# Kernel optimization log

Hardware: AMD Instinct MI355X
Metric: run time of the kernel (lower is better)

## Reference

```python
import jax, jax.numpy as jnp
import numpy as np

B, T, F_IN = 32, 2000, 256
HIDDEN, OUT = 1024, 256
TAU, DT, G = 0.01, 0.001, 1.2
HID_NOISE, OUT_NOISE = 0.05, 0.5
SPARSITY = 0.1


def setup_inputs() -> dict:
    key = jax.random.key(0)
    k_in, k_wr_n, k_wr_s, k_wi, k_wf, k_wo, k_xh, k_xo = jax.random.split(key, 8)
    inputs = jax.random.normal(k_in, (B, T, F_IN), dtype=jnp.float32)
    # recurrent kernel: sparse normal init (flax Dense kernel shape = (in, out))
    std = np.sqrt(1.0 / (SPARSITY * HIDDEN)).astype(np.float32)
    Wr = jax.random.normal(k_wr_n, (HIDDEN, HIDDEN), dtype=jnp.float32) * std
    Wr = Wr * jax.random.bernoulli(k_wr_s, 1.0 - SPARSITY, (HIDDEN, HIDDEN))
    # input and feedback kernels: uniform in [-1, 1)
    Wi = jax.random.uniform(k_wi, (F_IN, HIDDEN), dtype=jnp.float32, minval=-1.0, maxval=1.0)
    Wf = jax.random.uniform(k_wf, (OUT, HIDDEN), dtype=jnp.float32, minval=-1.0, maxval=1.0)
    # readout kernel (zeros_init in source; small random here for nontrivial signal)
    Wo = jax.random.normal(k_wo, (HIDDEN, OUT), dtype=jnp.float32) * 0.01
    # split_rngs={'reservoir': False} => same noise reused at every timestep
    xi_hidden = jax.random.uniform(k_xh, (B, HIDDEN), dtype=jnp.float32, minval=-HID_NOISE, maxval=HID_NOISE)
    xi_output = jax.random.uniform(k_xo, (B, OUT), dtype=jnp.float32, minval=-OUT_NOISE, maxval=OUT_NOISE)
    return {"inputs": inputs, "Wr": Wr, "Wi": Wi, "Wf": Wf, "Wo": Wo,
            "xi_hidden": xi_hidden, "xi_output": xi_output}


def reference(inputs, Wr, Wi, Wf, Wo, xi_hidden, xi_output):
    # inputs: [B, T, F_in]; scan over time with carry u: [B, H]
    x_t_first = jnp.swapaxes(inputs, 0, 1)  # [T, B, F_in]
    u0 = jnp.zeros((inputs.shape[0], Wr.shape[0]), dtype=inputs.dtype)

    def step(u, x):
        r = jnp.tanh(u) + xi_hidden                       # [B, H]
        z = r @ Wo + xi_output                            # [B, O]
        du = G * (r @ Wr) + x @ Wi + z @ Wf               # [B, H]
        u_new = u + DT * (du - u) / TAU                   # Euler update
        return u_new, z

    _, outputs = jax.lax.scan(step, u0, x_t_first)        # [T, B, O]
    return jnp.swapaxes(outputs, 0, 1)                    # [B, T, O]
```

## Files before the change

### kernel.cpp

```cpp
#include <hip/hip_runtime.h>
#include <math.h>

#define NB   32
#define NT   2000
#define NFIN 256
#define NH   1024
#define NOUT 256
#define KC   1280
#define GRID 256
#define BLK  256
#define HALF 128

#define WC_STR 12
#define OFF_WC   0
#define OFF_WOT  (OFF_WC + KC * WC_STR)
#define XS_STR   20
#define OFF_XS   (OFF_WOT + 2 * NH)
#define PD_STR   68
#define OFF_PD   (OFF_XS + NFIN * XS_STR)
#define LDS_FLOATS (OFF_PD + 160 * PD_STR)
#define LDS_BYTES  (LDS_FLOATS * 4)

__global__ __launch_bounds__(256) void init_wcomb(
    const float* __restrict__ Wr, const float* __restrict__ Wi,
    const float* __restrict__ Wf, const float* __restrict__ Wo,
    float* __restrict__ Wcb, float* __restrict__ Wot)
{
    __shared__ float wo_s[NOUT];
    const int k   = blockIdx.x;
    const int tid = threadIdx.x;
    float acc[4];
    if (k < NH) {
        wo_s[tid] = Wo[k * NOUT + tid];
        __syncthreads();
        Wot[(size_t)tid * NH + k] = wo_s[tid];
#pragma unroll
        for (int jj = 0; jj < 4; ++jj)
            acc[jj] = 1.2f * Wr[k * NH + jj * 256 + tid];
        for (int o = 0; o < NOUT; ++o) {
            const float w = wo_s[o];
#pragma unroll
            for (int jj = 0; jj < 4; ++jj)
                acc[jj] = fmaf(w, Wf[o * NH + jj * 256 + tid], acc[jj]);
        }
    } else {
        const int k2 = k - NH;
#pragma unroll
        for (int jj = 0; jj < 4; ++jj)
            acc[jj] = Wi[k2 * NH + jj * 256 + tid];
    }
#pragma unroll
    for (int jj = 0; jj < 4; ++jj) {
        const int j = jj * 256 + tid;
        Wcb[(size_t)(j >> 3) * (KC * 8) + k * 8 + (j & 7)] = acc[jj];
    }
}

__global__ __launch_bounds__(256) void init_state(
    const float* __restrict__ Wf, const float* __restrict__ xi_o,
    const float* __restrict__ xi_h,
    float* __restrict__ c_km, float* __restrict__ xih_km,
    float* __restrict__ r0, unsigned* __restrict__ bar)
{
    __shared__ float xo_s[NOUT];
    const int b   = blockIdx.x;
    const int tid = threadIdx.x;
    if (b == 0) bar[tid] = 0u;
    xo_s[tid] = xi_o[b * NOUT + tid];
    __syncthreads();
    float acc[4] = {0.f, 0.f, 0.f, 0.f};
    for (int o = 0; o < NOUT; ++o) {
        const float x = xo_s[o];
#pragma unroll
        for (int jj = 0; jj < 4; ++jj)
            acc[jj] = fmaf(x, Wf[o * NH + jj * 256 + tid], acc[jj]);
    }
#pragma unroll
    for (int jj = 0; jj < 4; ++jj) {
        const int j = jj * 256 + tid;
        const float xh = xi_h[b * NH + j];
        c_km[j * NB + b]   = acc[jj];
        xih_km[j * NB + b] = xh;
        r0[j * NB + b]     = xh;
    }
}

extern "C" __global__ __launch_bounds__(BLK, 1) void reservoir_persistent(
    const float* __restrict__ x_all,
    const float* __restrict__ Wcb,
    const float* __restrict__ Wot,
    const float* __restrict__ c_km,
    const float* __restrict__ xih_km,
    const float* __restrict__ xi_o,
    float* __restrict__ r0, float* __restrict__ r1,
    float* __restrict__ out,
    unsigned* __restrict__ bar)
{
    extern __shared__ float sm[];
    float* Wc_s  = sm + OFF_WC;
    float* Wot_s = sm + OFF_WOT;
    float* x_s   = sm + OFF_XS;
    float* pd    = sm + OFF_PD;

    const int tid = threadIdx.x;
    const int blk = blockIdx.x;
    const int bg  = blk & 1;
    const int cg  = blk >> 1;
    const int b0  = bg * 16;
    const int j0  = cg * 8;
    const int zc0 = cg * 2;

    unsigned* cnt = bar + (bg << 6);
    unsigned* flg = bar + 128 + (bg << 6);

#pragma unroll
    for (int i = 0; i < 10; ++i) {
        const int q = tid + BLK * i;
        const int k = q >> 1, h = q & 1;
        const float4 w = *(const float4*)&Wcb[(size_t)cg * (KC * 8) + k * 8 + h * 4];
        *(float4*)&Wc_s[k * WC_STR + h * 4] = w;
    }
#pragma unroll
    for (int i = 0; i < 8; ++i) {
        const int idx = tid + BLK * i;
        Wot_s[idx] = Wot[(size_t)zc0 * NH + idx];
    }

    float u_reg = 0.f, c_reg = 0.f, xih_reg = 0.f;
    int ep_addr = 0;
    if (tid < 128) {
        const int j = j0 + (tid >> 4);
        const int b = b0 + (tid & 15);
        ep_addr = j * NB + b;
        c_reg   = c_km[ep_addr];
        xih_reg = xih_km[ep_addr];
    }
    float zxi = 0.f; size_t z_out_base = 0;
    if (tid >= 128 && tid < 160) {
        const int o2 = tid - 128;
        const int zc = zc0 + (o2 >> 4);
        const int zb = b0 + (o2 & 15);
        zxi = xi_o[zb * NOUT + zc];
        z_out_base = (size_t)zb * NT * NOUT + zc;
    }

    const int ks5 = tid >> 2;
    const int bq  = tid & 3;
    const int bb  = tid & 15;
    const int q2  = tid >> 4;

    const float* rcur = r0;
    float*       rnxt = r1;

    {
        const float* xp = x_all + ((size_t)(b0 + bb) * NT + 0) * NFIN;
#pragma unroll
        for (int i = 0; i < 4; ++i) {
            const int kk = (q2 + 16 * i) * 4;
            const float4 v = *(const float4*)&xp[kk];
            x_s[(kk + 0) * XS_STR + bb] = v.x;
            x_s[(kk + 1) * XS_STR + bb] = v.y;
            x_s[(kk + 2) * XS_STR + bb] = v.z;
            x_s[(kk + 3) * XS_STR + bb] = v.w;
        }
    }
    __syncthreads();

    for (int t = 0; t < NT; ++t) {
        float ad[8][4], az[2][4];
#pragma unroll
        for (int jj = 0; jj < 8; ++jj)
#pragma unroll
            for (int i = 0; i < 4; ++i) ad[jj][i] = 0.f;
#pragma unroll
        for (int jq = 0; jq < 2; ++jq)
#pragma unroll
            for (int i = 0; i < 4; ++i) az[jq][i] = 0.f;

        const float* rbase = rcur + b0 + bq * 4;
        float4 rq4[16];
#pragma unroll
        for (int p = 0; p < 16; ++p)
            rq4[p] = *(const float4*)(rbase + (size_t)(ks5 + (p << 6)) * NB);

#pragma unroll
        for (int m = 0; m < 16; ++m) {
            const int k = ks5 + (m << 6);
            const float4 a = rq4[m];
            const float4 w0 = *(const float4*)&Wc_s[k * WC_STR];
            const float4 w1 = *(const float4*)&Wc_s[k * WC_STR + 4];
            const float z0 = Wot_s[k], z1 = Wot_s[NH + k];
            const float av[4] = {a.x, a.y, a.z, a.w};
            const float wv[8] = {w0.x, w0.y, w0.z, w0.w, w1.x, w1.y, w1.z, w1.w};
#pragma unroll
            for (int i = 0; i < 4; ++i) {
#pragma unroll
                for (int jj = 0; jj < 8; ++jj)
                    ad[jj][i] = fmaf(av[i], wv[jj], ad[jj][i]);
                az[0][i] = fmaf(av[i], z0, az[0][i]);
                az[1][i] = fmaf(av[i], z1, az[1][i]);
            }
        }
#pragma unroll
        for (int m = 0; m < 4; ++m) {
            const int kk = ks5 + (m << 6);
            const int k  = kk + NH;
            const float4 a  = *(const float4*)&x_s[kk * XS_STR + bq * 4];
            const float4 w0 = *(const float4*)&Wc_s[k * WC_STR];
            const float4 w1 = *(const float4*)&Wc_s[k * WC_STR + 4];
            const float av[4] = {a.x, a.y, a.z, a.w};
            const float wv[8] = {w0.x, w0.y, w0.z, w0.w, w1.x, w1.y, w1.z, w1.w};
#pragma unroll
            for (int i = 0; i < 4; ++i)
#pragma unroll
                for (int jj = 0; jj < 8; ++jj)
                    ad[jj][i] = fmaf(av[i], wv[jj], ad[jj][i]);
        }

        const int tn = (t + 1 < NT) ? (t + 1) : (NT - 1);
        float4 xv[4];
        {
            const float* xp = x_all + ((size_t)(b0 + bb) * NT + tn) * NFIN;
#pragma unroll
            for (int i = 0; i < 4; ++i)
                xv[i] = *(const float4*)&xp[(q2 + 16 * i) * 4];
        }

#pragma unroll
        for (int jj = 0; jj < 8; ++jj)
#pragma unroll
            for (int i = 0; i < 4; ++i)
                pd[(jj * 16 + bq * 4 + i) * PD_STR + ks5] = ad[jj][i];
#pragma unroll
        for (int jq = 0; jq < 2; ++jq)
#pragma unroll
            for (int i = 0; i < 4; ++i)
                pd[(128 + jq * 16 + bq * 4 + i) * PD_STR + ks5] = az[jq][i];
        __syncthreads();

        if (tid < 160) {
            const float* row = &pd[tid * PD_STR];
            float4 s4 = make_float4(0.f, 0.f, 0.f, 0.f);
#pragma unroll
            for (int q = 0; q < 16; ++q) {
                const float4 v = *(const float4*)&row[q * 4];
                s4.x += v.x; s4.y += v.y; s4.z += v.z; s4.w += v.w;
            }
            const float s = (s4.x + s4.y) + (s4.z + s4.w);
            if (tid < 128) {
                const float un = 0.9f * u_reg + 0.1f * (s + c_reg);
                u_reg = un;
                rnxt[ep_addr] = tanhf(un) + xih_reg;
            } else {
                out[z_out_base + (size_t)t * NOUT] = s + zxi;
            }
        }

        {
#pragma unroll
            for (int i = 0; i < 4; ++i) {
                const int kk = (q2 + 16 * i) * 4;
                const float4 v = xv[i];
                x_s[(kk + 0) * XS_STR + bb] = v.x;
                x_s[(kk + 1) * XS_STR + bb] = v.y;
                x_s[(kk + 2) * XS_STR + bb] = v.z;
                x_s[(kk + 3) * XS_STR + bb] = v.w;
            }
        }
        __syncthreads();

        if (tid == 0) {
            __builtin_amdgcn_fence(__ATOMIC_RELEASE, "agent");
            const unsigned tgt = (unsigned)HALF * (unsigned)(t + 1);
            const unsigned old = __hip_atomic_fetch_add(cnt, 1u, __ATOMIC_RELAXED,
                                                        __HIP_MEMORY_SCOPE_AGENT);
            if (old == tgt - 1u) {
                __hip_atomic_store(flg, tgt, __ATOMIC_RELAXED,
                                   __HIP_MEMORY_SCOPE_AGENT);
            } else {
                while (__hip_atomic_load(flg, __ATOMIC_RELAXED,
                                         __HIP_MEMORY_SCOPE_AGENT) < tgt)
                    __builtin_amdgcn_s_sleep(2);
            }
            __builtin_amdgcn_fence(__ATOMIC_ACQUIRE, "agent");
        }
        __syncthreads();

        float* tmp = (float*)rcur; rcur = rnxt; rnxt = tmp;
    }
}

extern "C" void kernel_launch(void* const* d_in, const int* in_sizes, int n_in,
                              void* d_out, int out_size, void* d_ws, size_t ws_size,
                              hipStream_t stream)
{
    const float* inputs = (const float*)d_in[0];
    const float* Wr     = (const float*)d_in[1];
    const float* Wi     = (const float*)d_in[2];
    const float* Wf     = (const float*)d_in[3];
    const float* Wo     = (const float*)d_in[4];
    const float* xi_h   = (const float*)d_in[5];
    const float* xi_o   = (const float*)d_in[6];
    float* out = (float*)d_out;

    float* ws     = (float*)d_ws;
    float* Wcb    = ws;
    float* Wot    = Wcb + 128 * KC * 8;
    float* c_km   = Wot + NOUT * NH;
    float* xih_km = c_km + NH * NB;
    float* r0     = xih_km + NH * NB;
    float* r1     = r0 + NH * NB;
    unsigned* bar = (unsigned*)(r1 + NH * NB);

    (void)hipFuncSetAttribute((const void*)reservoir_persistent,
                              hipFuncAttributeMaxDynamicSharedMemorySize, LDS_BYTES);

    init_wcomb<<<KC, 256, 0, stream>>>(Wr, Wi, Wf, Wo, Wcb, Wot);
    init_state<<<NB, 256, 0, stream>>>(Wf, xi_o, xi_h, c_km, xih_km, r0, bar);

    void* args[] = {
        (void*)&inputs, (void*)&Wcb, (void*)&Wot, (void*)&c_km, (void*)&xih_km,
        (void*)&xi_o, (void*)&r0, (void*)&r1, (void*)&out, (void*)&bar
    };
    (void)hipLaunchCooperativeKernel((void*)reservoir_persistent,
                                     dim3(GRID), dim3(BLK), args, LDS_BYTES, stream);
}
```

Before: 17.36 ms.

## Replace barrier fences with cache-bypassing loads/stores and pipeline r-chunk waits

Drops the agent-scope release/acquire fences around the grid barrier. Instead the shared r state is written and read with cache-bypassing (sc0 sc1) global instructions, and the counter/flag barrier is restructured so that any waiter can publish the flag. The r loads are issued up front and consumed in four chunks with staged vmcnt waits so compute overlaps the load latency. The x-part operands are prefetched into registers while the barrier is pending, and the Wot layout is interleaved so the two output weights come from one paired load. The fence removal relies on inline-asm cache bypass for correctness, which is fragile and may break memory ordering.

Result: slower. 20.07 ms (+15.6%).

```diff
diff --git a/kernel.cpp b/kernel.cpp
--- a/kernel.cpp
+++ b/kernel.cpp
@@ -10,6 +10,8 @@
 #define GRID 256
 #define BLK  256
 #define HALF 128
+
+typedef float f32x4 __attribute__((ext_vector_type(4)));
 
 #define WC_STR 12
 #define OFF_WC   0
@@ -123,7 +125,7 @@
 #pragma unroll
     for (int i = 0; i < 8; ++i) {
         const int idx = tid + BLK * i;
-        Wot_s[idx] = Wot[(size_t)zc0 * NH + idx];
+        Wot_s[((idx & 1023) << 1) | (idx >> 10)] = Wot[(size_t)zc0 * NH + idx];
     }
 
     float u_reg = 0.f, c_reg = 0.f, xih_reg = 0.f;
@@ -166,50 +168,71 @@
     }
     __syncthreads();
 
-    for (int t = 0; t < NT; ++t) {
-        float ad[8][4], az[2][4];
-#pragma unroll
-        for (int jj = 0; jj < 8; ++jj)
-#pragma unroll
-            for (int i = 0; i < 4; ++i) ad[jj][i] = 0.f;
-#pragma unroll
-        for (int jq = 0; jq < 2; ++jq)
-#pragma unroll
-            for (int i = 0; i < 4; ++i) az[jq][i] = 0.f;
-
-        const float* rbase = rcur + b0 + bq * 4;
-        float4 rq4[16];
-#pragma unroll
-        for (int p = 0; p < 16; ++p)
-            rq4[p] = *(const float4*)(rbase + (size_t)(ks5 + (p << 6)) * NB);
-
-#pragma unroll
-        for (int m = 0; m < 16; ++m) {
-            const int k = ks5 + (m << 6);
-            const float4 a = rq4[m];
-            const float4 w0 = *(const float4*)&Wc_s[k * WC_STR];
-            const float4 w1 = *(const float4*)&Wc_s[k * WC_STR + 4];
-            const float z0 = Wot_s[k], z1 = Wot_s[NH + k];
-            const float av[4] = {a.x, a.y, a.z, a.w};
-            const float wv[8] = {w0.x, w0.y, w0.z, w0.w, w1.x, w1.y, w1.z, w1.w};
-#pragma unroll
-            for (int i = 0; i < 4; ++i) {
-#pragma unroll
-                for (int jj = 0; jj < 8; ++jj)
-                    ad[jj][i] = fmaf(av[i], wv[jj], ad[jj][i]);
-                az[0][i] = fmaf(av[i], z0, az[0][i]);
-                az[1][i] = fmaf(av[i], z1, az[1][i]);
-            }
-        }
+    float4 xa[4], wx0[4], wx1[4];
+    auto prefetch_xpart = [&]() {
 #pragma unroll
         for (int m = 0; m < 4; ++m) {
             const int kk = ks5 + (m << 6);
-            const int k  = kk + NH;
-            const float4 a  = *(const float4*)&x_s[kk * XS_STR + bq * 4];
-            const float4 w0 = *(const float4*)&Wc_s[k * WC_STR];
-            const float4 w1 = *(const float4*)&Wc_s[k * WC_STR + 4];
-            const float av[4] = {a.x, a.y, a.z, a.w};
-            const float wv[8] = {w0.x, w0.y, w0.z, w0.w, w1.x, w1.y, w1.z, w1.w};
+            xa[m]  = *(const float4*)&x_s[kk * XS_STR + bq * 4];
+            wx0[m] = *(const float4*)&Wc_s[(kk + NH) * WC_STR];
+            wx1[m] = *(const float4*)&Wc_s[(kk + NH) * WC_STR + 4];
+        }
+    };
+    prefetch_xpart();
+
+    for (int t = 0; t < NT; ++t) {
+        const float* rbase = rcur + b0 + bq * 4;
+        f32x4 rq4[16];
+#pragma unroll
+        for (int p = 0; p < 16; ++p) {
+            const float* ap = rbase + (size_t)(ks5 + (p << 6)) * NB;
+            asm volatile("global_load_dwordx4 %0, %1, off sc0 sc1"
+                         : "=v"(rq4[p]) : "v"(ap));
+        }
+
+        float ad[8][4], az[2][4];
+#pragma unroll
+        for (int jj = 0; jj < 8; ++jj)
+#pragma unroll
+            for (int i = 0; i < 4; ++i) ad[jj][i] = 0.f;
+#pragma unroll
+        for (int jq = 0; jq < 2; ++jq)
+#pragma unroll
+            for (int i = 0; i < 4; ++i) az[jq][i] = 0.f;
+
+#define RCHUNK(M0, M1, VW)                                                     \
+        asm volatile("s_waitcnt vmcnt(" #VW ")" ::: "memory");                 \
+        __builtin_amdgcn_sched_barrier(0);                                     \
+        _Pragma("unroll")                                                      \
+        for (int m = M0; m < M1; ++m) {                                        \
+            const int k = ks5 + (m << 6);                                      \
+            const f32x4 a = rq4[m];                                            \
+            const float4 w0 = *(const float4*)&Wc_s[k * WC_STR];               \
+            const float4 w1 = *(const float4*)&Wc_s[k * WC_STR + 4];           \
+            const float2 zz = *(const float2*)&Wot_s[k * 2];                   \
+            const float av[4] = {a[0], a[1], a[2], a[3]};                      \
+            const float wv[8] = {w0.x, w0.y, w0.z, w0.w,                       \
+                                 w1.x, w1.y, w1.z, w1.w};                      \
+            _Pragma("unroll")                                                  \
+            for (int i = 0; i < 4; ++i) {                                      \
+                _Pragma("unroll")                                              \
+                for (int jj = 0; jj < 8; ++jj)                                 \
+                    ad[jj][i] = fmaf(av[i], wv[jj], ad[jj][i]);                \
+                az[0][i] = fmaf(av[i], zz.x, az[0][i]);                        \
+                az[1][i] = fmaf(av[i], zz.y, az[1][i]);                        \
+            }                                                                  \
+        }
+        RCHUNK(0, 4, 12)
+        RCHUNK(4, 8, 8)
+        RCHUNK(8, 12, 4)
+        RCHUNK(12, 16, 0)
+#undef RCHUNK
+
+#pragma unroll
+        for (int m = 0; m < 4; ++m) {
+            const float av[4] = {xa[m].x, xa[m].y, xa[m].z, xa[m].w};
+            const float wv[8] = {wx0[m].x, wx0[m].y, wx0[m].z, wx0[m].w,
+                                 wx1[m].x, wx1[m].y, wx1[m].z, wx1[m].w};
 #pragma unroll
             for (int i = 0; i < 4; ++i)
 #pragma unroll
@@ -250,11 +273,16 @@
             if (tid < 128) {
                 const float un = 0.9f * u_reg + 0.1f * (s + c_reg);
                 u_reg = un;
-                rnxt[ep_addr] = tanhf(un) + xih_reg;
+                const float rv = tanhf(un) + xih_reg;
+                const float* sp = rnxt + ep_addr;
+                asm volatile("global_store_dword %0, %1, off sc0 sc1"
+                             :: "v"(sp), "v"(rv) : "memory");
             } else {
                 out[z_out_base + (size_t)t * NOUT] = s + zxi;
             }
         }
+
+        asm volatile("s_waitcnt vmcnt(0)" ::: "memory");
 
         {
 #pragma unroll
@@ -269,20 +297,24 @@
         }
         __syncthreads();
 
+        if (tid == 0)
+            __hip_atomic_fetch_add(cnt, 1u, __ATOMIC_RELAXED,
+                                   __HIP_MEMORY_SCOPE_AGENT);
+
+        prefetch_xpart();
+
         if (tid == 0) {
-            __builtin_amdgcn_fence(__ATOMIC_RELEASE, "agent");
             const unsigned tgt = (unsigned)HALF * (unsigned)(t + 1);
-            const unsigned old = __hip_atomic_fetch_add(cnt, 1u, __ATOMIC_RELAXED,
-                                                        __HIP_MEMORY_SCOPE_AGENT);
-            if (old == tgt - 1u) {
-                __hip_atomic_store(flg, tgt, __ATOMIC_RELAXED,
-                                   __HIP_MEMORY_SCOPE_AGENT);
-            } else {
-                while (__hip_atomic_load(flg, __ATOMIC_RELAXED,
-                                         __HIP_MEMORY_SCOPE_AGENT) < tgt)
-                    __builtin_amdgcn_s_sleep(2);
+            while (__hip_atomic_load(flg, __ATOMIC_RELAXED,
+                                     __HIP_MEMORY_SCOPE_AGENT) < tgt) {
+                if (__hip_atomic_load(cnt, __ATOMIC_RELAXED,
+                                      __HIP_MEMORY_SCOPE_AGENT) >= tgt) {
+                    __hip_atomic_store(flg, tgt, __ATOMIC_RELAXED,
+                                       __HIP_MEMORY_SCOPE_AGENT);
+                    break;
+                }
+                __builtin_amdgcn_s_sleep(2);
             }
-            __builtin_amdgcn_fence(__ATOMIC_ACQUIRE, "agent");
         }
         __syncthreads();
 
```

## Replace flat grid barrier with two-level tree barrier and split arrive/wait

Applied to the files above, without the earlier changes.

Swaps the single-counter atomic barrier per batch group for a two-level tree: 16 leaf counters of 8 blocks each feed a root counter, which sets a flag. The hidden-state and output stores now use system-coherent (sc0 sc1) global stores followed by a vmcnt wait instead of a release fence, and the arrive is issued before the x_s staging, so that staging overlaps the barrier latency. This aims to cut atomic contention and barrier latency on the per-timestep grid sync. The risks are memory-ordering correctness relying on the cache-bypass stores, and a larger barrier-initialisation footprint.

New measurement: 17.84 ms. 1.03x slower.

```diff
diff --git a/kernel.cpp b/kernel.cpp
--- a/kernel.cpp
+++ b/kernel.cpp
@@ -65,7 +65,7 @@
     __shared__ float xo_s[NOUT];
     const int b   = blockIdx.x;
     const int tid = threadIdx.x;
-    if (b == 0) bar[tid] = 0u;
+    if (tid < 32) bar[b * 32 + tid] = 0u;
     xo_s[tid] = xi_o[b * NOUT + tid];
     __syncthreads();
     float acc[4] = {0.f, 0.f, 0.f, 0.f};
@@ -109,9 +109,11 @@
     const int b0  = bg * 16;
     const int j0  = cg * 8;
     const int zc0 = cg * 2;
-
-    unsigned* cnt = bar + (bg << 6);
-    unsigned* flg = bar + 128 + (bg << 6);
+    const int lf  = cg >> 3;
+
+    unsigned* leaf = bar + (bg << 9) + (lf << 4);
+    unsigned* root = bar + (bg << 9) + 256;
+    unsigned* flg  = bar + (bg << 9) + 272;
 
 #pragma unroll
     for (int i = 0; i < 10; ++i) {
@@ -250,9 +252,30 @@
             if (tid < 128) {
                 const float un = 0.9f * u_reg + 0.1f * (s + c_reg);
                 u_reg = un;
-                rnxt[ep_addr] = tanhf(un) + xih_reg;
+                const float rv = tanhf(un) + xih_reg;
+                const float* sp = rnxt + ep_addr;
+                asm volatile("global_store_dword %0, %1, off sc0 sc1"
+                             :: "v"(sp), "v"(rv) : "memory");
             } else {
-                out[z_out_base + (size_t)t * NOUT] = s + zxi;
+                const float zv = s + zxi;
+                const float* op = out + z_out_base + (size_t)t * NOUT;
+                asm volatile("global_store_dword %0, %1, off sc0 sc1"
+                             :: "v"(op), "v"(zv) : "memory");
+            }
+        }
+
+        asm volatile("s_waitcnt vmcnt(0)" ::: "memory");
+        __syncthreads();
+
+        if (tid == 0) {
+            const unsigned lo = __hip_atomic_fetch_add(leaf, 1u, __ATOMIC_RELAXED,
+                                                       __HIP_MEMORY_SCOPE_AGENT);
+            if (lo == 8u * (unsigned)(t + 1) - 1u) {
+                const unsigned ro = __hip_atomic_fetch_add(root, 1u, __ATOMIC_RELAXED,
+                                                           __HIP_MEMORY_SCOPE_AGENT);
+                if (ro == 16u * (unsigned)(t + 1) - 1u)
+                    __hip_atomic_store(flg, (unsigned)(t + 1), __ATOMIC_RELAXED,
+                                       __HIP_MEMORY_SCOPE_AGENT);
             }
         }
 
@@ -267,21 +290,11 @@
                 x_s[(kk + 3) * XS_STR + bb] = v.w;
             }
         }
-        __syncthreads();
 
         if (tid == 0) {
-            __builtin_amdgcn_fence(__ATOMIC_RELEASE, "agent");
-            const unsigned tgt = (unsigned)HALF * (unsigned)(t + 1);
-            const unsigned old = __hip_atomic_fetch_add(cnt, 1u, __ATOMIC_RELAXED,
-                                                        __HIP_MEMORY_SCOPE_AGENT);
-            if (old == tgt - 1u) {
-                __hip_atomic_store(flg, tgt, __ATOMIC_RELAXED,
-                                   __HIP_MEMORY_SCOPE_AGENT);
-            } else {
-                while (__hip_atomic_load(flg, __ATOMIC_RELAXED,
-                                         __HIP_MEMORY_SCOPE_AGENT) < tgt)
-                    __builtin_amdgcn_s_sleep(2);
-            }
+            while (__hip_atomic_load(flg, __ATOMIC_RELAXED,
+                                     __HIP_MEMORY_SCOPE_AGENT) < (unsigned)(t + 1))
+                __builtin_amdgcn_s_sleep(2);
             __builtin_amdgcn_fence(__ATOMIC_ACQUIRE, "agent");
         }
         __syncthreads();
```
